# Optimization experiments

Measured on AMD Instinct MI355X. Metric: run time of the kernel, lower is better.

The kernel has to match this reference:

```python
import jax, jax.numpy as jnp
import numpy as np

B, N, L = 32, 128, 1024
DRUG_DIM, TGT_DIM, HID, H = 256, 1280, 512, 8
HD = HID // H  # 64
NEG = jnp.float32(-1e9)


def setup_inputs() -> dict:
    key = jax.random.key(0)
    ks = jax.random.split(key, 9)
    drug_nodes = jax.random.normal(ks[0], (B, N, DRUG_DIM), dtype=jnp.float32)
    target_seq = jax.random.normal(ks[1], (B, L, TGT_DIM), dtype=jnp.float32)
    # masks: random valid lengths in [max//2, max], True = valid
    dlen = jax.random.randint(ks[2], (B,), N // 2, N + 1)
    tlen = jax.random.randint(ks[3], (B,), L // 2, L + 1)
    drug_mask = jnp.arange(N)[None, :] < dlen[:, None]
    target_mask = jnp.arange(L)[None, :] < tlen[:, None]
    # params (nn.Linear default init ~ U(-1/sqrt(fan_in), ...); randn*0.02 ok for a reference)
    Wd = jax.random.normal(ks[4], (DRUG_DIM, HID), dtype=jnp.float32) / np.sqrt(DRUG_DIM)
    bd = jnp.zeros((HID,), dtype=jnp.float32)
    Wt = jax.random.normal(ks[5], (TGT_DIM, HID), dtype=jnp.float32) / np.sqrt(TGT_DIM)
    bt = jnp.zeros((HID,), dtype=jnp.float32)
    Wb = jax.random.normal(ks[6], (H, HD, HD), dtype=jnp.float32) * 0.02
    return {"drug_nodes": drug_nodes, "drug_mask": drug_mask,
            "target_seq": target_seq, "target_mask": target_mask,
            "Wd": Wd, "bd": bd, "Wt": Wt, "bt": bt, "Wb": Wb}


def reference(drug_nodes, drug_mask, target_seq, target_mask, Wd, bd, Wt, bt, Wb):
    # project and split heads -> (h, B, n, hd) / (h, B, l, hd)
    d = drug_nodes @ Wd + bd                                  # (B, N, HID)
    t = target_seq @ Wt + bt                                  # (B, L, HID)
    dh = d.reshape(B, N, H, HD).transpose(2, 0, 1, 3)         # (H, B, N, HD)
    th = t.reshape(B, L, H, HD).transpose(2, 0, 1, 3)         # (H, B, L, HD)

    dW = jnp.einsum('hbnd,hde->hbne', dh, Wb)                 # bilinear map
    attn = jnp.einsum('hbne,hble->hbnl', dW, th)              # (H, B, N, L)

    mask = (drug_mask[:, :, None] & target_mask[:, None, :])[None]  # (1, B, N, L)
    scores = jnp.where(mask, attn, NEG)

    # drug-side softmax over protein residues (axis=-1), dropout is identity (eval)
    attn_d = jnp.where(mask, jax.nn.softmax(scores, axis=-1), 0.0)
    ctx_d = jnp.einsum('hbnl,hble->hbne', attn_d, th)         # (H, B, N, HD)
    dmf = drug_mask[None, :, :, None].astype(ctx_d.dtype)
    ctx_d = (ctx_d * dmf).sum(axis=2) / jnp.clip(dmf.sum(axis=2), 1.0)  # (H, B, HD)
    ctx_d = ctx_d.transpose(1, 0, 2).reshape(B, -1)           # (B, HID)

    # target-side softmax over atoms (axis=-2)
    attn_t = jnp.where(mask, jax.nn.softmax(scores, axis=-2), 0.0)
    ctx_t = jnp.einsum('hbnl,hbne->hble', attn_t, dh)         # (H, B, L, HD)
    tmf = target_mask[None, :, :, None].astype(ctx_t.dtype)
    ctx_t = (ctx_t * tmf).sum(axis=2) / jnp.clip(tmf.sum(axis=2), 1.0)  # (H, B, HD)
    ctx_t = ctx_t.transpose(1, 0, 2).reshape(B, -1)           # (B, HID)

    return jnp.concatenate([ctx_d, ctx_t], axis=-1)           # (B, 2*HID)
```

## Files before the change

### kernel.cpp

```cpp
#include <hip/hip_runtime.h>
#include <hip/hip_bf16.h>
#include <math.h>

#define B_ 32
#define N_ 128
#define L_ 1024
#define DD_ 256
#define TD_ 1280
#define HID_ 512
#define H_ 8
#define HD_ 64

#define WS_D    0
#define WS_RM   (WS_D   + 2097152)
#define WS_RIZ  (WS_RM  + 32768)
#define WS_RMT  (WS_RIZ + 32768)
#define WS_RZT  (WS_RMT + 524288)
#define WS_W    (WS_RZT + 524288)
#define WS_CNT  (WS_W   + 32768)
#define WS_WT   (WS_CNT + 64)
#define WS_THB  (WS_WT  + 327680)
#define WS_DWB  (WS_THB + 8388608)

using bf16x8 = __attribute__((ext_vector_type(8))) short;
using floatx4 = __attribute__((ext_vector_type(4))) float;

static __device__ __forceinline__ unsigned short f2bf(float f) {
  unsigned int u = __float_as_uint(f);
  unsigned int r = (u + 0x7FFFu + ((u >> 16) & 1u)) >> 16;
  return (unsigned short)r;
}
static __device__ __forceinline__ float bf2f(unsigned short s) {
  return __uint_as_float(((unsigned int)s) << 16);
}

__global__ __launch_bounds__(256) void count_kernel(const int* __restrict__ dmask,
                                                    const int* __restrict__ tmask,
                                                    int* __restrict__ cnts) {
  __shared__ int red[256];
  const int b = blockIdx.x, tid = threadIdx.x;
  const bool dint = (dmask[0] == 1);
  const bool tint = (tmask[0] == 1);
  int s = 0;
  if (dint) {
    for (int i = tid; i < N_; i += 256) s += (dmask[(size_t)b*N_ + i] != 0);
  } else {
    const unsigned char* p = (const unsigned char*)dmask;
    for (int i = tid; i < N_; i += 256) s += (p[(size_t)b*N_ + i] != 0);
  }
  red[tid] = s; __syncthreads();
  for (int off = 128; off > 0; off >>= 1) { if (tid < off) red[tid] += red[tid+off]; __syncthreads(); }
  if (tid == 0) cnts[b*2] = red[0];
  __syncthreads();
  s = 0;
  if (tint) {
    for (int i = tid; i < L_; i += 256) s += (tmask[(size_t)b*L_ + i] != 0);
  } else {
    const unsigned char* p = (const unsigned char*)tmask;
    for (int i = tid; i < L_; i += 256) s += (p[(size_t)b*L_ + i] != 0);
  }
  red[tid] = s; __syncthreads();
  for (int off = 128; off > 0; off >>= 1) { if (tid < off) red[tid] += red[tid+off]; __syncthreads(); }
  if (tid == 0) cnts[b*2+1] = red[0];
}

__global__ __launch_bounds__(256) void transpose_bf16_kernel(
    const float* __restrict__ W, unsigned short* __restrict__ WT, int K, int Nd) {
  __shared__ float tile[32][33];
  const int tid = threadIdx.x;
  const int n0 = blockIdx.x * 32, k0 = blockIdx.y * 32;
  const int c = tid & 31, r0 = tid >> 5;
#pragma unroll
  for (int i = 0; i < 4; i++) {
    const int r = r0 + i * 8;
    tile[c][r] = W[(size_t)(k0 + r) * Nd + n0 + c];
  }
  __syncthreads();
#pragma unroll
  for (int i = 0; i < 4; i++) {
    const int r = r0 + i * 8;
    WT[(size_t)(n0 + r) * K + k0 + c] = f2bf(tile[r][c]);
  }
}

__global__ __launch_bounds__(256) void gemm_t_mfma_kernel(
    const float* __restrict__ A, const unsigned short* __restrict__ WT,
    const float* __restrict__ bias, unsigned short* __restrict__ thb,
    int M, int K) {
  __shared__ __align__(16) unsigned short As[128 * 40];
  __shared__ __align__(16) unsigned short Bs[128 * 40];
  const int tid = threadIdx.x;
  const int lin = blockIdx.x;
  const int xcd = lin & 7, sq = lin >> 3;
  const int n_t = sq & 3, m_t = (sq >> 2) + xcd * 32;
  const int m0 = m_t * 128, n0 = n_t * 128;
  const int srow = tid >> 1, shalf = tid & 1;
  const int lane = tid & 63, wave = tid >> 6;
  const int wm = wave & 1, wn = wave >> 1;
  const int quad = lane >> 4, lrow = lane & 15;

  floatx4 acc[4][4];
#pragma unroll
  for (int i = 0; i < 4; i++)
#pragma unroll
    for (int j = 0; j < 4; j++) acc[i][j] = (floatx4){0.f, 0.f, 0.f, 0.f};

  const float* Aptr = A + (size_t)(m0 + srow) * K + shalf * 16;
  const unsigned short* Bptr = WT + (size_t)(n0 + srow) * K + shalf * 16;

  float4 a0 = *(const float4*)(Aptr + 0);
  float4 a1 = *(const float4*)(Aptr + 4);
  float4 a2 = *(const float4*)(Aptr + 8);
  float4 a3 = *(const float4*)(Aptr + 12);
  uint4 b0 = *(const uint4*)(Bptr + 0);
  uint4 b1 = *(const uint4*)(Bptr + 8);

  for (int k0 = 0; k0 < K; k0 += 32) {
    __syncthreads();
    {
      unsigned short* ap = &As[srow * 40 + shalf * 16];
      union { unsigned short s[8]; uint4 u; } pk;
      pk.s[0] = f2bf(a0.x); pk.s[1] = f2bf(a0.y); pk.s[2] = f2bf(a0.z); pk.s[3] = f2bf(a0.w);
      pk.s[4] = f2bf(a1.x); pk.s[5] = f2bf(a1.y); pk.s[6] = f2bf(a1.z); pk.s[7] = f2bf(a1.w);
      *(uint4*)ap = pk.u;
      pk.s[0] = f2bf(a2.x); pk.s[1] = f2bf(a2.y); pk.s[2] = f2bf(a2.z); pk.s[3] = f2bf(a2.w);
      pk.s[4] = f2bf(a3.x); pk.s[5] = f2bf(a3.y); pk.s[6] = f2bf(a3.z); pk.s[7] = f2bf(a3.w);
      *(uint4*)(ap + 8) = pk.u;
      unsigned short* bp = &Bs[srow * 40 + shalf * 16];
      *(uint4*)bp = b0;
      *(uint4*)(bp + 8) = b1;
    }
    __syncthreads();
    if (k0 + 32 < K) {
      a0 = *(const float4*)(Aptr + k0 + 32);
      a1 = *(const float4*)(Aptr + k0 + 36);
      a2 = *(const float4*)(Aptr + k0 + 40);
      a3 = *(const float4*)(Aptr + k0 + 44);
      b0 = *(const uint4*)(Bptr + k0 + 32);
      b1 = *(const uint4*)(Bptr + k0 + 40);
    }
    bf16x8 bfrag[4];
#pragma unroll
    for (int j = 0; j < 4; j++)
      bfrag[j] = *(const bf16x8*)&Bs[(wn * 64 + j * 16 + lrow) * 40 + quad * 8];
#pragma unroll
    for (int i = 0; i < 4; i++) {
      bf16x8 afrag = *(const bf16x8*)&As[(wm * 64 + i * 16 + lrow) * 40 + quad * 8];
#pragma unroll
      for (int j = 0; j < 4; j++)
        acc[i][j] = __builtin_amdgcn_mfma_f32_16x16x32_bf16(afrag, bfrag[j], acc[i][j], 0, 0, 0);
    }
  }

  float bj[4];
#pragma unroll
  for (int j = 0; j < 4; j++) bj[j] = bias[n0 + wn * 64 + j * 16 + lrow];
#pragma unroll
  for (int i = 0; i < 4; i++) {
#pragma unroll
    for (int j = 0; j < 4; j++) {
      const int gcol = n0 + wn * 64 + j * 16 + lrow;
      const int hh = gcol >> 6, e = gcol & 63;
#pragma unroll
      for (int r = 0; r < 4; r++) {
        const int grow = m0 + wm * 64 + i * 16 + quad * 4 + r;
        const int bb = grow >> 10, l = grow & 1023;
        thb[(((size_t)bb * H_ + hh) * L_ + l) * HD_ + e] = f2bf(acc[i][j][r] + bj[j]);
      }
    }
  }
}

__global__ __launch_bounds__(256) void gemm_bias_kernel(
    const float* __restrict__ A, const float* __restrict__ W,
    const float* __restrict__ bias, float* __restrict__ C,
    int M, int K, int Nd) {
  __shared__ float As[8][132];
  __shared__ float Bs[8][132];
  const int tid = threadIdx.x;
  const int m0 = blockIdx.y * 128, n0 = blockIdx.x * 128;
  const int lr = tid >> 1, lc = (tid & 1) * 4;
  const int wr = tid >> 5, wc = (tid & 31) * 4;
  const int tm = (tid >> 4) * 4, tn = (tid & 15) * 4;

  float acc[2][2][4][4];
#pragma unroll
  for (int a = 0; a < 2; a++)
#pragma unroll
    for (int bq = 0; bq < 2; bq++)
#pragma unroll
      for (int i = 0; i < 4; i++)
#pragma unroll
        for (int j = 0; j < 4; j++) acc[a][bq][i][j] = 0.f;

  const float* Aptr = A + (size_t)(m0 + lr) * K + lc;
  const float* Wptr = W + (size_t)wr * Nd + n0 + wc;

  for (int k0 = 0; k0 < K; k0 += 8) {
    float4 a4 = *(const float4*)(Aptr + k0);
    float4 w4 = *(const float4*)(Wptr + (size_t)k0 * Nd);
    __syncthreads();
    As[lc+0][lr] = a4.x; As[lc+1][lr] = a4.y; As[lc+2][lr] = a4.z; As[lc+3][lr] = a4.w;
    *(float4*)&Bs[wr][wc] = w4;
    __syncthreads();
#pragma unroll
    for (int kk = 0; kk < 8; kk++) {
      float4 a0 = *(const float4*)&As[kk][tm];
      float4 a1 = *(const float4*)&As[kk][tm + 64];
      float4 b0 = *(const float4*)&Bs[kk][tn];
      float4 b1 = *(const float4*)&Bs[kk][tn + 64];
      const float av0[4] = {a0.x, a0.y, a0.z, a0.w};
      const float av1[4] = {a1.x, a1.y, a1.z, a1.w};
      const float bv0[4] = {b0.x, b0.y, b0.z, b0.w};
      const float bv1[4] = {b1.x, b1.y, b1.z, b1.w};
#pragma unroll
      for (int i = 0; i < 4; i++)
#pragma unroll
        for (int j = 0; j < 4; j++) {
          acc[0][0][i][j] += av0[i] * bv0[j];
          acc[0][1][i][j] += av0[i] * bv1[j];
          acc[1][0][i][j] += av1[i] * bv0[j];
          acc[1][1][i][j] += av1[i] * bv1[j];
        }
    }
  }
  float4 bias0 = *(const float4*)&bias[n0 + tn];
  float4 bias1 = *(const float4*)&bias[n0 + tn + 64];
  const float bb0[4] = {bias0.x, bias0.y, bias0.z, bias0.w};
  const float bb1[4] = {bias1.x, bias1.y, bias1.z, bias1.w};
#pragma unroll
  for (int mh = 0; mh < 2; mh++)
#pragma unroll
    for (int i = 0; i < 4; i++) {
      const int row = m0 + mh * 64 + tm + i;
      float* cp = C + (size_t)row * Nd + n0;
      float4 o0, o1;
      o0.x = acc[mh][0][i][0] + bb0[0]; o0.y = acc[mh][0][i][1] + bb0[1];
      o0.z = acc[mh][0][i][2] + bb0[2]; o0.w = acc[mh][0][i][3] + bb0[3];
      o1.x = acc[mh][1][i][0] + bb1[0]; o1.y = acc[mh][1][i][1] + bb1[1];
      o1.z = acc[mh][1][i][2] + bb1[2]; o1.w = acc[mh][1][i][3] + bb1[3];
      *(float4*)(cp + tn) = o0;
      *(float4*)(cp + tn + 64) = o1;
    }
}

__global__ __launch_bounds__(256) void dw_kernel(
    const float* __restrict__ dproj, const float* __restrict__ Wb,
    unsigned short* __restrict__ dWb) {
  __shared__ float wb_s[64 * 64];
  const int tid = threadIdx.x;
  const int hb = blockIdx.x, b = hb >> 3, h = hb & 7;
  for (int i = tid; i < 4096; i += 256) wb_s[i] = Wb[(size_t)h * 4096 + i];
  __syncthreads();
  const int n = tid >> 1, half = tid & 1;
  float acc[32];
#pragma unroll
  for (int e = 0; e < 32; e++) acc[e] = 0.f;
  const float* dpr = dproj + ((size_t)(b * N_ + n)) * HID_ + h * HD_;
  for (int k = 0; k < 64; k++) {
    const float a = dpr[k];
    const float* wr = &wb_s[k * 64 + half * 32];
#pragma unroll
    for (int e = 0; e < 32; e++) acc[e] += a * wr[e];
  }
  unsigned short* outp = dWb + ((size_t)hb * N_ + n) * HD_ + half * 32;
#pragma unroll
  for (int e = 0; e < 32; e++) outp[e] = f2bf(acc[e]);
}

__device__ __forceinline__ void mfma_S_tile(
    const unsigned short* __restrict__ thp, const unsigned short* __restrict__ dwp,
    float* __restrict__ S_s, int ncnt, int lv, int tid) {
  const int lane = tid & 63, wave = tid >> 6;
  const int quad = lane >> 4, lr = lane & 15;
  const int noff = (wave & 1) * 64, loff = (wave >> 1) * 32;

  floatx4 acc[4][2];
#pragma unroll
  for (int i = 0; i < 4; i++)
#pragma unroll
    for (int j = 0; j < 2; j++) acc[i][j] = (floatx4){0.f, 0.f, 0.f, 0.f};

#pragma unroll
  for (int kc = 0; kc < 2; kc++) {
    bf16x8 bfr[2];
#pragma unroll
    for (int j = 0; j < 2; j++)
      bfr[j] = *(const bf16x8*)&thp[(size_t)(loff + j * 16 + lr) * HD_ + kc * 32 + quad * 8];
#pragma unroll
    for (int i = 0; i < 4; i++) {
      bf16x8 afr = *(const bf16x8*)&dwp[(size_t)(noff + i * 16 + lr) * HD_ + kc * 32 + quad * 8];
#pragma unroll
      for (int j = 0; j < 2; j++)
        acc[i][j] = __builtin_amdgcn_mfma_f32_16x16x32_bf16(afr, bfr[j], acc[i][j], 0, 0, 0);
    }
  }
#pragma unroll
  for (int i = 0; i < 4; i++)
#pragma unroll
    for (int j = 0; j < 2; j++)
#pragma unroll
      for (int r = 0; r < 4; r++) {
        const int n = noff + i * 16 + quad * 4 + r;
        const int li = loff + j * 16 + lr;
        const bool ok = (n < ncnt) && (li < lv);
        S_s[n * 69 + li] = ok ? acc[i][j][r] : -1e9f;
      }
}

__global__ __launch_bounds__(256, 4) void attn_stats_kernel(
    const unsigned short* __restrict__ thb, const unsigned short* __restrict__ dWb,
    const int* __restrict__ cnts, float* __restrict__ w_g,
    float* __restrict__ rmt, float* __restrict__ rzt) {
  __shared__ float S_s[128 * 69];
  __shared__ float red[256];
  __shared__ float zb_s[256], wb_s[256];
  __shared__ float cm_s[64], ics_s[64];
  const int tid = threadIdx.x;
  const int hb = blockIdx.x >> 4, lt = blockIdx.x & 15;
  const int b = hb >> 3;
  const int ncnt = cnts[b * 2], lcnt = cnts[b * 2 + 1];
  const int l0g = lt * 64;
  if (l0g >= lcnt) return;
  const int lv = min(64, lcnt - l0g);

  mfma_S_tile(thb + ((size_t)hb * L_ + l0g) * HD_, dWb + (size_t)hb * N_ * HD_,
              S_s, ncnt, lv, tid);
  __syncthreads();

  {
    const int l = tid & 63, q = tid >> 6;
    float pm = -INFINITY;
    for (int n = q * 32; n < q * 32 + 32; n++) pm = fmaxf(pm, S_s[n * 69 + l]);
    red[tid] = pm;
  }
  __syncthreads();
  if (tid < 64)
    cm_s[tid] = fmaxf(fmaxf(red[tid], red[tid + 64]), fmaxf(red[tid + 128], red[tid + 192]));
  __syncthreads();
  {
    const int l = tid & 63, q = tid >> 6;
    const float cm = cm_s[l];
    float ps = 0.f;
    for (int n = q * 32; n < q * 32 + 32; n++) ps += __expf(S_s[n * 69 + l] - cm);
    red[tid] = ps;
  }
  __syncthreads();
  if (tid < 64)
    ics_s[tid] = 1.f / (red[tid] + red[tid + 64] + red[tid + 128] + red[tid + 192]);
  __syncthreads();
  {
    const int n = tid & 127, half = tid >> 7;
    const float* Sr = &S_s[n * 69];
    const int lb = half * 32, le = min(lb + 32, lv);
    float tmax = -INFINITY;
    for (int l = lb; l < le; l++) tmax = fmaxf(tmax, Sr[l]);
    red[tid] = tmax;
    __syncthreads();
    const float tm = fmaxf(red[n], red[n + 128]);
    float z = 0.f, w = 0.f;
    for (int l = lb; l < le; l++) {
      const float s = Sr[l];
      z += __expf(s - tm);
      w += __expf(s - cm_s[l]) * ics_s[l];
    }
    zb_s[tid] = z; wb_s[tid] = w;
    __syncthreads();
    if (tid < 128) {
      rmt[((size_t)hb * 16 + lt) * 128 + tid] = tm;
      rzt[((size_t)hb * 16 + lt) * 128 + tid] = zb_s[tid] + zb_s[tid + 128];
      const float wsum = wb_s[tid] + wb_s[tid + 128];
      if (wsum != 0.f) atomicAdd(&w_g[hb * 128 + tid], wsum);
    }
  }
}

__global__ __launch_bounds__(256) void attn_combine_kernel(
    const float* __restrict__ rmt, const float* __restrict__ rzt,
    const float* __restrict__ w_g, const float* __restrict__ dproj,
    const int* __restrict__ cnts, float* __restrict__ rm_g,
    float* __restrict__ riz_g, float* __restrict__ outp) {
  __shared__ float red[256];
  const int tid = threadIdx.x;
  const int hb = blockIdx.x, b = hb >> 3, h = hb & 7;
  const int ncnt = cnts[b * 2], lcnt = cnts[b * 2 + 1];
  const int ntl = (lcnt + 63) >> 6;
  if (tid < 128) {
    const int n = tid;
    float m = -INFINITY;
    for (int t = 0; t < ntl; t++)
      m = fmaxf(m, rmt[((size_t)hb * 16 + t) * 128 + n]);
    float Z = 0.f;
    for (int t = 0; t < ntl; t++)
      Z += rzt[((size_t)hb * 16 + t) * 128 + n] * __expf(rmt[((size_t)hb * 16 + t) * 128 + n] - m);
    rm_g[hb * 128 + n] = m;
    riz_g[hb * 128 + n] = (n < ncnt) ? 1.f / Z : 0.f;
  }
  const int e = tid & 63, q = tid >> 6;
  float p = 0.f;
  const int nb = q * 32, ne = min(nb + 32, ncnt);
  for (int n = nb; n < ne; n++)
    p += w_g[hb * 128 + n] * dproj[((size_t)(b * N_ + n)) * HID_ + h * HD_ + e];
  red[tid] = p;
  __syncthreads();
  if (tid < 64) {
    const float s = red[tid] + red[tid + 64] + red[tid + 128] + red[tid + 192];
    outp[(size_t)b * (2 * HID_) + HID_ + h * HD_ + tid] = s / (float)lcnt;
  }
}

__global__ __launch_bounds__(256, 4) void attn_v_kernel(
    const unsigned short* __restrict__ thb, const unsigned short* __restrict__ dWb,
    const int* __restrict__ cnts, const float* __restrict__ rm_g,
    const float* __restrict__ riz_g, float* __restrict__ outp) {
  __shared__ float S_s[128 * 69];
  __shared__ float red[256];
  __shared__ float rm_s[128], riz_s[128], v_s[64];
  const int tid = threadIdx.x;
  const int hb = blockIdx.x >> 4, lt = blockIdx.x & 15;
  const int b = hb >> 3, h = hb & 7;
  const int ncnt = cnts[b * 2], lcnt = cnts[b * 2 + 1];
  const int l0g = lt * 64;
  if (l0g >= lcnt) return;
  const int lv = min(64, lcnt - l0g);

  if (tid < 128) {
    rm_s[tid] = rm_g[hb * 128 + tid];
    riz_s[tid] = riz_g[hb * 128 + tid];
  }
  const unsigned short* thp = thb + ((size_t)hb * L_ + l0g) * HD_;
  mfma_S_tile(thp, dWb + (size_t)hb * N_ * HD_, S_s, ncnt, lv, tid);
  __syncthreads();

  {
    const int l = tid & 63, q = tid >> 6;
    float vp = 0.f;
    for (int n = q * 32; n < q * 32 + 32; n++)
      vp += __expf(S_s[n * 69 + l] - rm_s[n]) * riz_s[n];
    red[tid] = vp;
  }
  __syncthreads();
  const float incnt = 1.f / (float)ncnt;
  if (tid < 64) {
    const float v = (tid < lv)
        ? (red[tid] + red[tid + 64] + red[tid + 128] + red[tid + 192]) * incnt
        : 0.f;
    v_s[tid] = v;
  }
  __syncthreads();
  {
    const int e = tid & 63, q = tid >> 6;
    float p = 0.f;
    for (int l = q * 16; l < q * 16 + 16; l++)
      p += v_s[l] * bf2f(thp[(size_t)l * HD_ + e]);
    red[tid] = p;
  }
  __syncthreads();
  if (tid < 64) {
    const float s = red[tid] + red[tid + 64] + red[tid + 128] + red[tid + 192];
    if (s != 0.f)
      atomicAdd(&outp[(size_t)b * (2 * HID_) + h * HD_ + tid], s);
  }
}

extern "C" void kernel_launch(void* const* d_in, const int* in_sizes, int n_in,
                              void* d_out, int out_size, void* d_ws, size_t ws_size,
                              hipStream_t stream) {
  const float* drug = (const float*)d_in[0];
  const int* dmask = (const int*)d_in[1];
  const float* tseq = (const float*)d_in[2];
  const int* tmask = (const int*)d_in[3];
  const float* Wd = (const float*)d_in[4];
  const float* bd = (const float*)d_in[5];
  const float* Wt = (const float*)d_in[6];
  const float* bt = (const float*)d_in[7];
  const float* Wb = (const float*)d_in[8];
  float* out = (float*)d_out;
  float* ws = (float*)d_ws;

  float* dp = ws + WS_D;
  float* rm = ws + WS_RM;
  float* riz = ws + WS_RIZ;
  float* rmt = ws + WS_RMT;
  float* rzt = ws + WS_RZT;
  float* w_g = ws + WS_W;
  int* cnts = (int*)(ws + WS_CNT);
  unsigned short* wtT = (unsigned short*)(ws + WS_WT);
  unsigned short* thb = (unsigned short*)(ws + WS_THB);
  unsigned short* dWb = (unsigned short*)(ws + WS_DWB);

  count_kernel<<<B_, 256, 0, stream>>>(dmask, tmask, cnts);
  hipMemsetAsync(w_g, 0, (size_t)(B_ * H_ * N_) * sizeof(float), stream);
  hipMemsetAsync(out, 0, (size_t)out_size * sizeof(float), stream);
  transpose_bf16_kernel<<<dim3(HID_ / 32, TD_ / 32), 256, 0, stream>>>(Wt, wtT, TD_, HID_);
  gemm_t_mfma_kernel<<<(HID_ / 128) * ((B_ * L_) / 128), 256, 0, stream>>>(
      tseq, wtT, bt, thb, B_ * L_, TD_);
  gemm_bias_kernel<<<dim3(HID_ / 128, (B_ * N_) / 128), 256, 0, stream>>>(
      drug, Wd, bd, dp, B_ * N_, DD_, HID_);
  dw_kernel<<<B_ * H_, 256, 0, stream>>>(dp, Wb, dWb);
  attn_stats_kernel<<<B_ * H_ * 16, 256, 0, stream>>>(thb, dWb, cnts, w_g, rmt, rzt);
  attn_combine_kernel<<<B_ * H_, 256, 0, stream>>>(rmt, rzt, w_g, dp, cnts, rm, riz, out);
  attn_v_kernel<<<B_ * H_ * 16, 256, 0, stream>>>(thb, dWb, cnts, rm, riz, out);
}
```

Baseline: 486.5 us.

## Pre-convert target sequence to bf16 and stage GEMM tiles via direct global-to-LDS loads

Adds a separate kernel that converts the fp32 target sequence to bf16 once. The projection GEMM then loads bf16 tiles straight into LDS with global_load_lds, using an XOR-swizzled layout and a K step of 64 in place of register staging with in-loop conversion. It also replaces the atomic accumulation of per-row weights with per-tile partial buffers that the combine kernel reduces, which removes one memset and the atomics. The cost is an extra full pass over the 168MB input plus a 84MB bf16 copy, and the new GEMM loop no longer prefetches the next tile during the MFMAs.

```diff
diff --git a/kernel.cpp b/kernel.cpp
--- a/kernel.cpp
+++ b/kernel.cpp
@@ -16,11 +16,12 @@
 #define WS_RIZ  (WS_RM  + 32768)
 #define WS_RMT  (WS_RIZ + 32768)
 #define WS_RZT  (WS_RMT + 524288)
-#define WS_W    (WS_RZT + 524288)
-#define WS_CNT  (WS_W   + 32768)
+#define WS_RWT  (WS_RZT + 524288)
+#define WS_CNT  (WS_RWT + 524288)
 #define WS_WT   (WS_CNT + 64)
 #define WS_THB  (WS_WT  + 327680)
 #define WS_DWB  (WS_THB + 8388608)
+#define WS_ABF  (WS_DWB + 1048576)
 
 using bf16x8 = __attribute__((ext_vector_type(8))) short;
 using floatx4 = __attribute__((ext_vector_type(4))) float;
@@ -32,6 +33,11 @@
 }
 static __device__ __forceinline__ float bf2f(unsigned short s) {
   return __uint_as_float(((unsigned int)s) << 16);
+}
+static __device__ __forceinline__ void gload16(const void* g, void* l) {
+  __builtin_amdgcn_global_load_lds(
+      (const __attribute__((address_space(1))) void*)g,
+      (__attribute__((address_space(3))) void*)l, 16, 0, 0);
 }
 
 __global__ __launch_bounds__(256) void count_kernel(const int* __restrict__ dmask,
@@ -64,6 +70,21 @@
   if (tid == 0) cnts[b*2+1] = red[0];
 }
 
+__global__ __launch_bounds__(256) void a2bf_kernel(const float* __restrict__ A,
+                                                   unsigned short* __restrict__ Abf,
+                                                   long n) {
+  long i = ((long)blockIdx.x * 256 + threadIdx.x) * 8;
+  const long stride = (long)gridDim.x * 256 * 8;
+  for (; i < n; i += stride) {
+    float4 x = *(const float4*)(A + i);
+    float4 y = *(const float4*)(A + i + 4);
+    union { unsigned short s[8]; uint4 u; } p;
+    p.s[0] = f2bf(x.x); p.s[1] = f2bf(x.y); p.s[2] = f2bf(x.z); p.s[3] = f2bf(x.w);
+    p.s[4] = f2bf(y.x); p.s[5] = f2bf(y.y); p.s[6] = f2bf(y.z); p.s[7] = f2bf(y.w);
+    *(uint4*)(Abf + i) = p.u;
+  }
+}
+
 __global__ __launch_bounds__(256) void transpose_bf16_kernel(
     const float* __restrict__ W, unsigned short* __restrict__ WT, int K, int Nd) {
   __shared__ float tile[32][33];
@@ -84,17 +105,15 @@
 }
 
 __global__ __launch_bounds__(256) void gemm_t_mfma_kernel(
-    const float* __restrict__ A, const unsigned short* __restrict__ WT,
-    const float* __restrict__ bias, unsigned short* __restrict__ thb,
-    int M, int K) {
-  __shared__ __align__(16) unsigned short As[128 * 40];
-  __shared__ __align__(16) unsigned short Bs[128 * 40];
+    const unsigned short* __restrict__ Abf, const unsigned short* __restrict__ WT,
+    const float* __restrict__ bias, unsigned short* __restrict__ thb, int K) {
+  __shared__ __align__(16) unsigned short As[8192];
+  __shared__ __align__(16) unsigned short Bs[8192];
   const int tid = threadIdx.x;
   const int lin = blockIdx.x;
   const int xcd = lin & 7, sq = lin >> 3;
   const int n_t = sq & 3, m_t = (sq >> 2) + xcd * 32;
   const int m0 = m_t * 128, n0 = n_t * 128;
-  const int srow = tid >> 1, shalf = tid & 1;
   const int lane = tid & 63, wave = tid >> 6;
   const int wm = wave & 1, wn = wave >> 1;
   const int quad = lane >> 4, lrow = lane & 15;
@@ -105,50 +124,46 @@
 #pragma unroll
     for (int j = 0; j < 4; j++) acc[i][j] = (floatx4){0.f, 0.f, 0.f, 0.f};
 
-  const float* Aptr = A + (size_t)(m0 + srow) * K + shalf * 16;
-  const unsigned short* Bptr = WT + (size_t)(n0 + srow) * K + shalf * 16;
-
-  float4 a0 = *(const float4*)(Aptr + 0);
-  float4 a1 = *(const float4*)(Aptr + 4);
-  float4 a2 = *(const float4*)(Aptr + 8);
-  float4 a3 = *(const float4*)(Aptr + 12);
-  uint4 b0 = *(const uint4*)(Bptr + 0);
-  uint4 b1 = *(const uint4*)(Bptr + 8);
-
-  for (int k0 = 0; k0 < K; k0 += 32) {
+  int srcoff[2][2];
+#pragma unroll
+  for (int call = 0; call < 2; call++) {
+    const int i = call * 256 + tid;
+    const int r = i >> 2;
+    const int c = (i & 3) ^ ((r >> 1) & 3);
+#pragma unroll
+    for (int g = 0; g < 2; g++) srcoff[call][g] = r * K + g * 32 + c * 8;
+  }
+  const unsigned short* Abase = Abf + (size_t)m0 * K;
+  const unsigned short* Bbase = WT + (size_t)n0 * K;
+
+  for (int k0 = 0; k0 < K; k0 += 64) {
     __syncthreads();
-    {
-      unsigned short* ap = &As[srow * 40 + shalf * 16];
-      union { unsigned short s[8]; uint4 u; } pk;
-      pk.s[0] = f2bf(a0.x); pk.s[1] = f2bf(a0.y); pk.s[2] = f2bf(a0.z); pk.s[3] = f2bf(a0.w);
-      pk.s[4] = f2bf(a1.x); pk.s[5] = f2bf(a1.y); pk.s[6] = f2bf(a1.z); pk.s[7] = f2bf(a1.w);
-      *(uint4*)ap = pk.u;
-      pk.s[0] = f2bf(a2.x); pk.s[1] = f2bf(a2.y); pk.s[2] = f2bf(a2.z); pk.s[3] = f2bf(a2.w);
-      pk.s[4] = f2bf(a3.x); pk.s[5] = f2bf(a3.y); pk.s[6] = f2bf(a3.z); pk.s[7] = f2bf(a3.w);
-      *(uint4*)(ap + 8) = pk.u;
-      unsigned short* bp = &Bs[srow * 40 + shalf * 16];
-      *(uint4*)bp = b0;
-      *(uint4*)(bp + 8) = b1;
+#pragma unroll
+    for (int g = 0; g < 2; g++) {
+#pragma unroll
+      for (int call = 0; call < 2; call++) {
+        const int dst = g * 4096 + (call * 256 + wave * 64) * 8;
+        gload16(Abase + k0 + srcoff[call][g], &As[dst]);
+        gload16(Bbase + k0 + srcoff[call][g], &Bs[dst]);
+      }
     }
     __syncthreads();
-    if (k0 + 32 < K) {
-      a0 = *(const float4*)(Aptr + k0 + 32);
-      a1 = *(const float4*)(Aptr + k0 + 36);
-      a2 = *(const float4*)(Aptr + k0 + 40);
-      a3 = *(const float4*)(Aptr + k0 + 44);
-      b0 = *(const uint4*)(Bptr + k0 + 32);
-      b1 = *(const uint4*)(Bptr + k0 + 40);
-    }
-    bf16x8 bfrag[4];
-#pragma unroll
-    for (int j = 0; j < 4; j++)
-      bfrag[j] = *(const bf16x8*)&Bs[(wn * 64 + j * 16 + lrow) * 40 + quad * 8];
-#pragma unroll
-    for (int i = 0; i < 4; i++) {
-      bf16x8 afrag = *(const bf16x8*)&As[(wm * 64 + i * 16 + lrow) * 40 + quad * 8];
-#pragma unroll
-      for (int j = 0; j < 4; j++)
-        acc[i][j] = __builtin_amdgcn_mfma_f32_16x16x32_bf16(afrag, bfrag[j], acc[i][j], 0, 0, 0);
+#pragma unroll
+    for (int g = 0; g < 2; g++) {
+      bf16x8 bfr[4];
+#pragma unroll
+      for (int j = 0; j < 4; j++) {
+        const int br = wn * 64 + j * 16 + lrow;
+        bfr[j] = *(const bf16x8*)&Bs[g * 4096 + (br * 4 + (quad ^ ((br >> 1) & 3))) * 8];
+      }
+#pragma unroll
+      for (int i = 0; i < 4; i++) {
+        const int ar = wm * 64 + i * 16 + lrow;
+        bf16x8 afr = *(const bf16x8*)&As[g * 4096 + (ar * 4 + (quad ^ ((ar >> 1) & 3))) * 8];
+#pragma unroll
+        for (int j = 0; j < 4; j++)
+          acc[i][j] = __builtin_amdgcn_mfma_f32_16x16x32_bf16(afr, bfr[j], acc[i][j], 0, 0, 0);
+      }
     }
   }
 
@@ -310,7 +325,7 @@
 
 __global__ __launch_bounds__(256, 4) void attn_stats_kernel(
     const unsigned short* __restrict__ thb, const unsigned short* __restrict__ dWb,
-    const int* __restrict__ cnts, float* __restrict__ w_g,
+    const int* __restrict__ cnts, float* __restrict__ rwt,
     float* __restrict__ rmt, float* __restrict__ rzt) {
   __shared__ float S_s[128 * 69];
   __shared__ float red[256];
@@ -367,20 +382,21 @@
     zb_s[tid] = z; wb_s[tid] = w;
     __syncthreads();
     if (tid < 128) {
-      rmt[((size_t)hb * 16 + lt) * 128 + tid] = tm;
-      rzt[((size_t)hb * 16 + lt) * 128 + tid] = zb_s[tid] + zb_s[tid + 128];
-      const float wsum = wb_s[tid] + wb_s[tid + 128];
-      if (wsum != 0.f) atomicAdd(&w_g[hb * 128 + tid], wsum);
+      const size_t o = ((size_t)hb * 16 + lt) * 128 + tid;
+      rmt[o] = tm;
+      rzt[o] = zb_s[tid] + zb_s[tid + 128];
+      rwt[o] = wb_s[tid] + wb_s[tid + 128];
     }
   }
 }
 
 __global__ __launch_bounds__(256) void attn_combine_kernel(
     const float* __restrict__ rmt, const float* __restrict__ rzt,
-    const float* __restrict__ w_g, const float* __restrict__ dproj,
+    const float* __restrict__ rwt, const float* __restrict__ dproj,
     const int* __restrict__ cnts, float* __restrict__ rm_g,
     float* __restrict__ riz_g, float* __restrict__ outp) {
   __shared__ float red[256];
+  __shared__ float w_s[128];
   const int tid = threadIdx.x;
   const int hb = blockIdx.x, b = hb >> 3, h = hb & 7;
   const int ncnt = cnts[b * 2], lcnt = cnts[b * 2 + 1];
@@ -390,17 +406,22 @@
     float m = -INFINITY;
     for (int t = 0; t < ntl; t++)
       m = fmaxf(m, rmt[((size_t)hb * 16 + t) * 128 + n]);
-    float Z = 0.f;
-    for (int t = 0; t < ntl; t++)
-      Z += rzt[((size_t)hb * 16 + t) * 128 + n] * __expf(rmt[((size_t)hb * 16 + t) * 128 + n] - m);
+    float Z = 0.f, w = 0.f;
+    for (int t = 0; t < ntl; t++) {
+      const size_t o = ((size_t)hb * 16 + t) * 128 + n;
+      Z += rzt[o] * __expf(rmt[o] - m);
+      w += rwt[o];
+    }
     rm_g[hb * 128 + n] = m;
     riz_g[hb * 128 + n] = (n < ncnt) ? 1.f / Z : 0.f;
-  }
+    w_s[n] = (n < ncnt) ? w : 0.f;
+  }
+  __syncthreads();
   const int e = tid & 63, q = tid >> 6;
   float p = 0.f;
   const int nb = q * 32, ne = min(nb + 32, ncnt);
   for (int n = nb; n < ne; n++)
-    p += w_g[hb * 128 + n] * dproj[((size_t)(b * N_ + n)) * HID_ + h * HD_ + e];
+    p += w_s[n] * dproj[((size_t)(b * N_ + n)) * HID_ + h * HD_ + e];
   red[tid] = p;
   __syncthreads();
   if (tid < 64) {
@@ -483,22 +504,23 @@
   float* riz = ws + WS_RIZ;
   float* rmt = ws + WS_RMT;
   float* rzt = ws + WS_RZT;
-  float* w_g = ws + WS_W;
+  float* rwt = ws + WS_RWT;
   int* cnts = (int*)(ws + WS_CNT);
   unsigned short* wtT = (unsigned short*)(ws + WS_WT);
   unsigned short* thb = (unsigned short*)(ws + WS_THB);
   unsigned short* dWb = (unsigned short*)(ws + WS_DWB);
+  unsigned short* abf = (unsigned short*)(ws + WS_ABF);
 
   count_kernel<<<B_, 256, 0, stream>>>(dmask, tmask, cnts);
-  hipMemsetAsync(w_g, 0, (size_t)(B_ * H_ * N_) * sizeof(float), stream);
   hipMemsetAsync(out, 0, (size_t)out_size * sizeof(float), stream);
+  a2bf_kernel<<<1024, 256, 0, stream>>>(tseq, abf, (long)B_ * L_ * TD_);
   transpose_bf16_kernel<<<dim3(HID_ / 32, TD_ / 32), 256, 0, stream>>>(Wt, wtT, TD_, HID_);
   gemm_t_mfma_kernel<<<(HID_ / 128) * ((B_ * L_) / 128), 256, 0, stream>>>(
-      tseq, wtT, bt, thb, B_ * L_, TD_);
+      abf, wtT, bt, thb, TD_);
   gemm_bias_kernel<<<dim3(HID_ / 128, (B_ * N_) / 128), 256, 0, stream>>>(
       drug, Wd, bd, dp, B_ * N_, DD_, HID_);
   dw_kernel<<<B_ * H_, 256, 0, stream>>>(dp, Wb, dWb);
-  attn_stats_kernel<<<B_ * H_ * 16, 256, 0, stream>>>(thb, dWb, cnts, w_g, rmt, rzt);
-  attn_combine_kernel<<<B_ * H_, 256, 0, stream>>>(rmt, rzt, w_g, dp, cnts, rm, riz, out);
+  attn_stats_kernel<<<B_ * H_ * 16, 256, 0, stream>>>(thb, dWb, cnts, rwt, rmt, rzt);
+  attn_combine_kernel<<<B_ * H_, 256, 0, stream>>>(rmt, rzt, rwt, dp, cnts, rm, riz, out);
   attn_v_kernel<<<B_ * H_ * 16, 256, 0, stream>>>(thb, dWb, cnts, rm, riz, out);
 }
```

New measurement: 472.1 us. -3.0%, faster.
